# Kernel tuning notes

Hardware: AMD Instinct MI355X
Metric: run time of the kernel (lower is better)

The kernel has to match this reference:

```python
import jax, jax.numpy as jnp
import numpy as np

B, IN_DIM, SIZE = 1024, 64, 2048
D1, D2 = 64, 64  # hidden_dims=[64], out_dim=64 (depth=2, linspace default)
NEG_SLOPE = 0.2


def setup_inputs() -> dict:
    key = jax.random.key(0)
    ks = jax.random.split(key, 5)
    x = jax.random.normal(ks[0], (B, IN_DIM), dtype=jnp.float32)
    # conv_0: Conv1d(1, size*d1, kernel=in_dim) weight (size*d1, 1, in_dim) -> (size, d1, in_dim)
    W0 = jax.random.normal(ks[1], (SIZE, D1, IN_DIM), dtype=jnp.float32) * (1.0 / np.sqrt(IN_DIM))
    b0 = jax.random.normal(ks[2], (SIZE, D1), dtype=jnp.float32) * 0.01
    # conv_1: Conv1d(size, size*d2, kernel=d1, groups=size) weight (size*d2, 1, d1) -> (size, d2, d1)
    W1 = jax.random.normal(ks[3], (SIZE, D2, D1), dtype=jnp.float32) * (1.0 / np.sqrt(D1))
    b1 = jax.random.normal(ks[4], (SIZE, D2), dtype=jnp.float32) * 0.01
    return {"x": x, "W0": W0, "b0": b0, "W1": W1, "b1": b1}


def reference(x, W0, b0, W1, b1):
    # Layer 0: full-length Conv1d over 1 input channel == dense linear broadcast over groups.
    # h[b,g,j] = sum_k W0[g,j,k] * x[b,k] + b0[g,j]
    h = jnp.einsum('bk,gjk->bgj', x, W0) + b0  # (B, SIZE, D1)
    h = jnp.where(h > 0, h, NEG_SLOPE * h)     # LeakyReLU(0.2)
    # Layer 1: grouped full-length Conv1d == independent per-group linear maps.
    # out[b,g,j] = sum_k W1[g,j,k] * h[b,g,k] + b1[g,j]
    out = jnp.einsum('bgk,gjk->bgj', h, W1) + b1  # (B, SIZE, D2)
    return out
```

## Files before the change

kernel.cpp:

```cpp
#include <hip/hip_runtime.h>

#define BATCH 1024
#define NGRP  2048
#define DIM   64
#define NEG   0.2f
#define OUTSTRIDE ((size_t)NGRP * DIM)

typedef __attribute__((ext_vector_type(8)))  short bf16x8;
typedef __attribute__((ext_vector_type(4)))  short short4v;
typedef __attribute__((ext_vector_type(16))) float f32x16;

union frag_u { bf16x8 v; unsigned u[4]; short4v h[2]; };

__device__ __forceinline__ unsigned pk_rne(float a, float b) {
    unsigned ua = __float_as_uint(a), ub = __float_as_uint(b);
    ua += 0x7fffu + ((ua >> 16) & 1u);
    ub += 0x7fffu + ((ub >> 16) & 1u);
    return __builtin_amdgcn_perm(ub, ua, 0x07060302);
}

__global__ void cvt_x_kernel(const float4* __restrict__ x, uint2* __restrict__ xb) {
    int i = blockIdx.x * blockDim.x + threadIdx.x;
    float4 v = x[i];
    uint2 o;
    o.x = pk_rne(v.x, v.y);
    o.y = pk_rne(v.z, v.w);
    xb[i] = o;
}

__global__ __launch_bounds__(256, 3)
void convnn_kernel(const unsigned short* __restrict__ xb,
                   const float* __restrict__ W0, const float* __restrict__ b0,
                   const float* __restrict__ W1, const float* __restrict__ b1,
                   float* __restrict__ out) {
    __shared__ short hs[4][32][68];

    const int g    = blockIdx.x;
    const int tid  = threadIdx.x;
    const int lane = tid & 63;
    const int wave = tid >> 6;
    const int n    = lane & 31;
    const int koff = (lane >> 5) * 8;

    frag_u w0f[4][2], w1f[4][2];
    {
        const float* w0p = W0 + (size_t)g * DIM * DIM;
        const float* w1p = W1 + (size_t)g * DIM * DIM;
        #pragma unroll
        for (int kk = 0; kk < 4; ++kk) {
            #pragma unroll
            for (int p = 0; p < 2; ++p) {
                const float* r0 = w0p + (size_t)(2 * n + p) * DIM + kk * 16 + koff;
                float4 lo = *(const float4*)r0;
                float4 hi = *(const float4*)(r0 + 4);
                w0f[kk][p].u[0] = pk_rne(lo.x, lo.y);
                w0f[kk][p].u[1] = pk_rne(lo.z, lo.w);
                w0f[kk][p].u[2] = pk_rne(hi.x, hi.y);
                w0f[kk][p].u[3] = pk_rne(hi.z, hi.w);
                const float* r1 = w1p + (size_t)(2 * n + p) * DIM + kk * 16 + koff;
                float4 lo1 = *(const float4*)r1;
                float4 hi1 = *(const float4*)(r1 + 4);
                w1f[kk][p].u[0] = pk_rne(lo1.x, lo1.y);
                w1f[kk][p].u[1] = pk_rne(lo1.z, lo1.w);
                w1f[kk][p].u[2] = pk_rne(hi1.x, hi1.y);
                w1f[kk][p].u[3] = pk_rne(hi1.z, hi1.w);
            }
        }
    }
    const float2 b0v = *(const float2*)(b0 + (size_t)g * DIM + 2 * n);
    const float2 b1v = *(const float2*)(b1 + (size_t)g * DIM + 2 * n);

    short (*h)[68] = hs[wave];

    bf16x8 a[4];
    {
        int tb = wave * 32;
        const unsigned short* xr = xb + (size_t)(tb + n) * DIM + koff;
        #pragma unroll
        for (int kk = 0; kk < 4; ++kk) a[kk] = *(const bf16x8*)(xr + kk * 16);
    }

    for (int i = 0; i < 8; ++i) {
        const int tb = (i * 4 + wave) * 32;
        bf16x8 an[4];
        {
            int tn = ((i < 7 ? i + 1 : 7) * 4 + wave) * 32;
            const unsigned short* xr = xb + (size_t)(tn + n) * DIM + koff;
            #pragma unroll
            for (int kk = 0; kk < 4; ++kk) an[kk] = *(const bf16x8*)(xr + kk * 16);
        }

        f32x16 aE, aO;
        #pragma unroll
        for (int r = 0; r < 16; ++r) { aE[r] = 0.f; aO[r] = 0.f; }
        #pragma unroll
        for (int kk = 0; kk < 4; ++kk) {
            aE = __builtin_amdgcn_mfma_f32_32x32x16_bf16(a[kk], w0f[kk][0].v, aE, 0, 0, 0);
            aO = __builtin_amdgcn_mfma_f32_32x32x16_bf16(a[kk], w0f[kk][1].v, aO, 0, 0, 0);
        }
        #pragma unroll
        for (int r = 0; r < 16; ++r) {
            int m = (r & 3) + 8 * (r >> 2) + 4 * (lane >> 5);
            float vE = aE[r] + b0v.x; vE = vE > 0.f ? vE : NEG * vE;
            float vO = aO[r] + b0v.y; vO = vO > 0.f ? vO : NEG * vO;
            *(unsigned*)&h[m][2 * n] = pk_rne(vE, vO);
        }

        f32x16 cE, cO;
        #pragma unroll
        for (int r = 0; r < 16; ++r) { cE[r] = 0.f; cO[r] = 0.f; }
        #pragma unroll
        for (int kk = 0; kk < 4; ++kk) {
            frag_u hf;
            hf.h[0] = *(const short4v*)&h[n][kk * 16 + koff];
            hf.h[1] = *(const short4v*)&h[n][kk * 16 + koff + 4];
            cE = __builtin_amdgcn_mfma_f32_32x32x16_bf16(hf.v, w1f[kk][0].v, cE, 0, 0, 0);
            cO = __builtin_amdgcn_mfma_f32_32x32x16_bf16(hf.v, w1f[kk][1].v, cO, 0, 0, 0);
        }

        float* ob = out + (size_t)tb * OUTSTRIDE + (size_t)g * DIM + 2 * n;
        #pragma unroll
        for (int r = 0; r < 16; ++r) {
            int m = (r & 3) + 8 * (r >> 2) + 4 * (lane >> 5);
            float2 o2;
            o2.x = cE[r] + b1v.x;
            o2.y = cO[r] + b1v.y;
            *(float2*)(ob + (size_t)m * OUTSTRIDE) = o2;
        }

        #pragma unroll
        for (int kk = 0; kk < 4; ++kk) a[kk] = an[kk];
    }
}

extern "C" void kernel_launch(void* const* d_in, const int* in_sizes, int n_in,
                              void* d_out, int out_size, void* d_ws, size_t ws_size,
                              hipStream_t stream) {
    const float* x  = (const float*)d_in[0];
    const float* W0 = (const float*)d_in[1];
    const float* b0 = (const float*)d_in[2];
    const float* W1 = (const float*)d_in[3];
    const float* b1 = (const float*)d_in[4];
    float* out = (float*)d_out;
    unsigned short* xb = (unsigned short*)d_ws;

    cvt_x_kernel<<<dim3(64), dim3(256), 0, stream>>>((const float4*)x, (uint2*)xb);
    convnn_kernel<<<dim3(NGRP), dim3(256), 0, stream>>>(xb, W0, b0, W1, b1, out);
}
```

Measured before the change: 605.3 us.

## Stage outputs of 8 groups in LDS for contiguous 2KB row stores

Each block now handles 8 groups (one per wave) over half the batch, instead of one group over the whole batch. Each wave writes its 32x64 output tile to shared memory. After a barrier, the block stores full 2KB contiguous rows of the output with float4 writes, replacing scattered 256-byte float2 segments. This targets write coalescing on the 512MB output, which dominates cost, at the price of two block-wide barriers per iteration and a larger LDS footprint (64KB plus the h buffer), which may limit occupancy.

Measured after the change: 615.8 us. About the same (+1.7%).

```diff
diff --git a/kernel.cpp b/kernel.cpp
--- a/kernel.cpp
+++ b/kernel.cpp
@@ -5,6 +5,10 @@
 #define DIM   64
 #define NEG   0.2f
 #define OUTSTRIDE ((size_t)NGRP * DIM)
+
+#define G_PER_BLK 8
+#define B_PER_BLK 512
+#define ITERS     (B_PER_BLK / 32)
 
 typedef __attribute__((ext_vector_type(8)))  short bf16x8;
 typedef __attribute__((ext_vector_type(4)))  short short4v;
@@ -28,19 +32,23 @@
     xb[i] = o;
 }
 
-__global__ __launch_bounds__(256, 3)
+__global__ __launch_bounds__(512, 2)
 void convnn_kernel(const unsigned short* __restrict__ xb,
                    const float* __restrict__ W0, const float* __restrict__ b0,
                    const float* __restrict__ W1, const float* __restrict__ b1,
                    float* __restrict__ out) {
-    __shared__ short hs[4][32][68];
+    __shared__ short hs[8][32][68];
+    __shared__ float sl[32][G_PER_BLK * DIM];
 
-    const int g    = blockIdx.x;
+    const int bx   = blockIdx.x;
+    const int gs   = bx & 255;
+    const int bh   = bx >> 8;
     const int tid  = threadIdx.x;
     const int lane = tid & 63;
     const int wave = tid >> 6;
     const int n    = lane & 31;
     const int koff = (lane >> 5) * 8;
+    const int g    = gs * G_PER_BLK + wave;
 
     frag_u w0f[4][2], w1f[4][2];
     {
@@ -71,20 +79,20 @@
     const float2 b1v = *(const float2*)(b1 + (size_t)g * DIM + 2 * n);
 
     short (*h)[68] = hs[wave];
+    const int tb0 = bh * B_PER_BLK;
 
     bf16x8 a[4];
     {
-        int tb = wave * 32;
-        const unsigned short* xr = xb + (size_t)(tb + n) * DIM + koff;
+        const unsigned short* xr = xb + (size_t)(tb0 + n) * DIM + koff;
         #pragma unroll
         for (int kk = 0; kk < 4; ++kk) a[kk] = *(const bf16x8*)(xr + kk * 16);
     }
 
-    for (int i = 0; i < 8; ++i) {
-        const int tb = (i * 4 + wave) * 32;
+    for (int i = 0; i < ITERS; ++i) {
+        const int tb = tb0 + i * 32;
         bf16x8 an[4];
         {
-            int tn = ((i < 7 ? i + 1 : 7) * 4 + wave) * 32;
+            int tn = tb0 + (i < ITERS - 1 ? i + 1 : i) * 32;
             const unsigned short* xr = xb + (size_t)(tn + n) * DIM + koff;
             #pragma unroll
             for (int kk = 0; kk < 4; ++kk) an[kk] = *(const bf16x8*)(xr + kk * 16);
@@ -118,15 +126,30 @@
             cO = __builtin_amdgcn_mfma_f32_32x32x16_bf16(hf.v, w1f[kk][1].v, cO, 0, 0, 0);
         }
 
-        float* ob = out + (size_t)tb * OUTSTRIDE + (size_t)g * DIM + 2 * n;
         #pragma unroll
         for (int r = 0; r < 16; ++r) {
             int m = (r & 3) + 8 * (r >> 2) + 4 * (lane >> 5);
             float2 o2;
             o2.x = cE[r] + b1v.x;
             o2.y = cO[r] + b1v.y;
-            *(float2*)(ob + (size_t)m * OUTSTRIDE) = o2;
+            *(float2*)&sl[m][wave * DIM + 2 * n] = o2;
         }
+
+        __syncthreads();
+
+        {
+            const int u     = tid & 127;
+            const int rbase = tid >> 7;
+            #pragma unroll
+            for (int j = 0; j < 8; ++j) {
+                int r = j * 4 + rbase;
+                float4 v = *(const float4*)&sl[r][u * 4];
+                *(float4*)(out + (size_t)(tb + r) * OUTSTRIDE
+                               + (size_t)gs * (G_PER_BLK * DIM) + u * 4) = v;
+            }
+        }
+
+        __syncthreads();
 
         #pragma unroll
         for (int kk = 0; kk < 4; ++kk) a[kk] = an[kk];
@@ -145,5 +168,5 @@
     unsigned short* xb = (unsigned short*)d_ws;
 
     cvt_x_kernel<<<dim3(64), dim3(256), 0, stream>>>((const float4*)x, (uint2*)xb);
-    convnn_kernel<<<dim3(NGRP), dim3(256), 0, stream>>>(xb, W0, b0, W1, b1, out);
+    convnn_kernel<<<dim3(512), dim3(512), 0, stream>>>(xb, W0, b0, W1, b1, out);
 }
```
